# Kernel tuning notes

Hardware: AMD Instinct MI355X
Metric: run time of the kernel (lower is better)

## Reference

```python
import jax, jax.numpy as jnp
import numpy as np

B, Z, H, W, C = 1, 8, 60, 120, 192
HEADS = 6
HD = C // HEADS
WS = (2, 6, 12)
SS = (1, 3, 6)  # window_size//2 shifts
LAM = False
N = WS[0] * WS[1] * WS[2]  # 144 tokens per window
nZ, nH, nL = Z // WS[0], H // WS[1], W // WS[2]
TYPES = nZ * nH            # earth-specific bias window types (pl,lat absolute)
EPS = 1e-5


def _position_index():
    # Pangu earth-specific relative index: lon relative, pl/lat absolute pairs
    wz, wh, ww = WS
    c1 = np.stack(np.meshgrid(np.arange(wz), np.arange(wh), np.arange(ww), indexing='ij')).reshape(3, -1)
    c2 = np.stack(np.meshgrid(-np.arange(wz) * wz, -np.arange(wh) * wh, np.arange(ww), indexing='ij')).reshape(3, -1)
    d = (c1[:, :, None] - c2[:, None, :]).transpose(1, 2, 0)
    d[..., 2] += ww - 1
    d[..., 1] *= 2 * ww - 1
    d[..., 0] *= (2 * ww - 1) * wh * wh
    return d.sum(-1)  # (N, N)


def _attn_mask():
    # Swin-3D shifted-window mask; lon is periodic on the sphere (lam=False) -> unmasked
    img = np.zeros((Z, H, W), np.int32)
    def segs(w, s, masked):
        return [slice(0, -w), slice(-w, -s), slice(-s, None)] if masked else [slice(None)]
    cnt = 0
    for zs in segs(WS[0], SS[0], True):
        for hs in segs(WS[1], SS[1], True):
            for ls in segs(WS[2], SS[2], LAM):
                img[zs, hs, ls] = cnt
                cnt += 1
    m = img.reshape(nZ, WS[0], nH, WS[1], nL, WS[2]).transpose(0, 2, 4, 1, 3, 5).reshape(-1, N)
    return np.where(m[:, None, :] != m[:, :, None], -100.0, 0.0).astype(np.float32)  # (nZ*nH*nL, N, N)


POS_IDX = _position_index()
MASK = jnp.asarray(_attn_mask().reshape(TYPES, nL, 1, N, N))


def _layernorm(x, g, b):
    mu = x.mean(-1, keepdims=True)
    var = ((x - mu) ** 2).mean(-1, keepdims=True)
    return (x - mu) * jax.lax.rsqrt(var + EPS) * g + b


def setup_inputs() -> dict:
    key = jax.random.key(0)
    ks = jax.random.split(key, 8)
    f = lambda k, shape: jax.random.normal(k, shape, jnp.float32) * 0.02
    return {
        'x': jax.random.normal(ks[0], (B, Z * H * W, C), jnp.float32),
        'cond_embed': jax.random.normal(ks[1], (B, 6 * C), jnp.float32) * 0.1,
        'g1': jnp.ones((C,), jnp.float32), 'bt1': jnp.zeros((C,), jnp.float32),
        'w_qkv': f(ks[2], (C, 3 * C)), 'b_qkv': jnp.zeros((3 * C,), jnp.float32),
        'bias_table': f(ks[3], ((2 * WS[2] - 1) * WS[1] ** 2 * WS[0] ** 2, TYPES, HEADS)),
        'w_proj': f(ks[4], (C, C)), 'b_proj': jnp.zeros((C,), jnp.float32),
        'g2': jnp.ones((C,), jnp.float32), 'bt2': jnp.zeros((C,), jnp.float32),
        'w_fc1': f(ks[5], (C, 4 * C)), 'b_fc1': jnp.zeros((4 * C,), jnp.float32),
        'w_fc2': f(ks[6], (4 * C, C)), 'b_fc2': jnp.zeros((C,), jnp.float32),
    }


def reference(x, cond_embed, g1, bt1, w_qkv, b_qkv, bias_table, w_proj, b_proj,
              g2, bt2, w_fc1, b_fc1, w_fc2, b_fc2):
    shortcut = x
    sh_msa, sc_msa, gt_msa, sh_mlp, sc_mlp, gt_mlp = jnp.split(cond_embed, 6, axis=1)
    h = _layernorm(x, g1, bt1)
    h = h * (1 + sc_msa[:, None, :]) + sh_msa[:, None, :]          # AdaLN modulate
    h = h.reshape(B, Z, H, W, C)
    h = jnp.roll(h, (-SS[0], -SS[1], -SS[2]), axis=(1, 2, 3))     # shifted window
    # window partition -> (B*nZ*nH*nL, N, C)
    hw = h.reshape(B, nZ, WS[0], nH, WS[1], nL, WS[2], C)
    hw = hw.transpose(0, 1, 3, 5, 2, 4, 6, 7).reshape(-1, N, C)
    qkv = (hw @ w_qkv + b_qkv).reshape(-1, N, 3, HEADS, HD)
    q, k, v = qkv[:, :, 0], qkv[:, :, 1], qkv[:, :, 2]
    attn = jnp.einsum('bnhd,bmhd->bhnm', q * (HD ** -0.5), k)      # (B_, heads, N, N)
    bias = bias_table[POS_IDX].transpose(2, 3, 0, 1)               # (types, heads, N, N)
    attn = attn.reshape(B, TYPES, nL, HEADS, N, N)
    attn = attn + bias[None, :, None] + MASK[None]
    attn = jax.nn.softmax(attn, axis=-1).reshape(-1, HEADS, N, N)
    out = jnp.einsum('bhnm,bmhd->bnhd', attn, v).reshape(-1, N, C)
    out = out @ w_proj + b_proj
    # reverse window partition + roll back
    h = out.reshape(B, nZ, nH, nL, WS[0], WS[1], WS[2], C)
    h = h.transpose(0, 1, 4, 2, 5, 3, 6, 7).reshape(B, Z, H, W, C)
    h = jnp.roll(h, (SS[0], SS[1], SS[2]), axis=(1, 2, 3)).reshape(B, Z * H * W, C)
    y = shortcut + gt_msa[:, None, :] * h
    mlp_in = _layernorm(y, g2, bt2) * (1 + sc_mlp[:, None, :]) + sh_mlp[:, None, :]
    mlp_out = jax.nn.gelu(mlp_in @ w_fc1 + b_fc1, approximate=False) @ w_fc2 + b_fc2
    return y + gt_mlp[:, None, :] * mlp_out
```

## Files before the change

kernel.cpp:

```cpp
#include <hip/hip_runtime.h>
#include <hip/hip_bf16.h>
#include <cmath>

typedef short short8 __attribute__((ext_vector_type(8)));
typedef short short4v __attribute__((ext_vector_type(4)));
typedef float f32x4 __attribute__((ext_vector_type(4)));
typedef __hip_bfloat16 bf16;

static __device__ __forceinline__ float bf2f(bf16 v) { return __bfloat162float(v); }
static __device__ __forceinline__ bf16 f2bf(float v) { return __float2bfloat16(v); }
static __device__ __forceinline__ short bfbits(float v) {
    bf16 t = f2bf(v); return *reinterpret_cast<short*>(&t);
}
static __device__ __forceinline__ float sbits2f(short s) {
    unsigned int u = ((unsigned int)(unsigned short)s) << 16;
    float f; __builtin_memcpy(&f, &u, 4); return f;
}
static __device__ __forceinline__ float ldin(const void* p, size_t i, bool f32) {
    return f32 ? reinterpret_cast<const float*>(p)[i]
               : bf2f(reinterpret_cast<const bf16*>(p)[i]);
}
static __device__ __forceinline__ bool sniff_f32(const void* g1) {
    return reinterpret_cast<const unsigned short*>(g1)[0] == 0;
}

__global__ __launch_bounds__(256) void k_pre(
    const void* __restrict__ w0, const void* __restrict__ w1,
    const void* __restrict__ w2, const void* __restrict__ w3,
    bf16* __restrict__ Bt,
    const void* __restrict__ x, const void* __restrict__ cond,
    const void* __restrict__ g1, const void* __restrict__ bt1,
    bf16* __restrict__ hw, const void* __restrict__ btab,
    bf16* __restrict__ bm)
{
    bool f32 = sniff_f32(g1);
    int bb = blockIdx.x, tid = threadIdx.x;
    if (bb < 1728) {
        int e = bb * 256 + tid;
        const void* W; bf16* dst; int i, N, K;
        if (e < 110592)        { W = w0; dst = Bt;          i = e;          N = 576; K = 192; }
        else if (e < 147456)   { W = w1; dst = Bt + 110592; i = e - 110592; N = 192; K = 192; }
        else if (e < 294912)   { W = w2; dst = Bt + 147456; i = e - 147456; N = 768; K = 192; }
        else                   { W = w3; dst = Bt + 294912; i = e - 294912; N = 192; K = 768; }
        int k = i / N, n = i % N;
        dst[(size_t)n * K + k] = f2bf(ldin(W, i, f32));
        return;
    }
    if (bb < 1968) {
        int tb = bb - 1728;
        int type = tb / 6, head = tb % 6;
        int iz = type / 10, ih = type % 10;
        bf16* out = bm + (size_t)tb * 20736;
        for (int e = tid; e < 20736; e += 256) {
            int r = e & 3, l = (e >> 2) & 63, f = e >> 8;
            int nt = f % 9, w = f / 9;
            int i = w * 16 + (l >> 4) * 4 + r, j = nt * 16 + (l & 15);
            int a1 = i / 72, b1 = (i / 12) % 6, c1 = i % 12;
            int a2 = j / 72, b2 = (j / 12) % 6, c2 = j % 12;
            int pidx = ((a1 + 2 * a2) * 36 + (b1 + 6 * b2)) * 23 + (c1 - c2 + 11);
            float b = ldin(btab, (size_t)pidx * 240 + type * 6 + head, f32);
            int zi = iz * 2 + a1, hi = ih * 6 + b1;
            int zj = iz * 2 + a2, hj = ih * 6 + b2;
            int ri = (zi < 6 ? 0 : (zi < 7 ? 1 : 2)) * 3 + (hi < 54 ? 0 : (hi < 57 ? 1 : 2));
            int rj = (zj < 6 ? 0 : (zj < 7 ? 1 : 2)) * 3 + (hj < 54 ? 0 : (hj < 57 ? 1 : 2));
            if (ri != rj) b -= 100.0f;
            out[e] = f2bf(b);
        }
        return;
    }
    int t = (bb - 1968) * 4 + (tid >> 6);
    int lane = tid & 63;
    float v[3];
#pragma unroll
    for (int e = 0; e < 3; e++) v[e] = ldin(x, (size_t)t * 192 + lane + 64 * e, f32);
    float s = v[0] + v[1] + v[2];
#pragma unroll
    for (int off = 32; off; off >>= 1) s += __shfl_xor(s, off);
    float mu = s * (1.0f / 192.0f);
    float sq = 0.f;
#pragma unroll
    for (int e = 0; e < 3; e++) { float d = v[e] - mu; sq += d * d; }
#pragma unroll
    for (int off = 32; off; off >>= 1) sq += __shfl_xor(sq, off);
    float rs = rsqrtf(sq * (1.0f / 192.0f) + 1e-5f);

    int z = t / 7200, rem = t % 7200, hy = rem / 120, wx = rem % 120;
    int zr = (z + 7) & 7, hr = (hy + 57) % 60, wr = (wx + 114) % 120;
    int widx = ((zr >> 1) * 10 + hr / 6) * 10 + wr / 12;
    int n = ((zr & 1) * 6 + hr % 6) * 12 + wr % 12;
    bf16* dst = hw + ((size_t)widx * 144 + n) * 192;
#pragma unroll
    for (int e = 0; e < 3; e++) {
        int c = lane + 64 * e;
        float hv = (v[e] - mu) * rs * ldin(g1, c, f32) + ldin(bt1, c, f32);
        float o = hv * (1.0f + ldin(cond, 192 + c, f32)) + ldin(cond, c, f32);
        dst[c] = f2bf(o);
    }
}

__global__ __launch_bounds__(256) void k_gemm4(
    const bf16* __restrict__ A, const bf16* __restrict__ Bt,
    const void* __restrict__ bias, void* __restrict__ C,
    int Mrows, int N, int K,
    const void* __restrict__ g1)
{
    __shared__ short Bs[64 * 200];
    bool f32 = sniff_f32(g1);
    int tid = threadIdx.x;
    int wave = tid >> 6, lane = tid & 63, col16 = lane & 15, quad = lane >> 4;
    int nbase = blockIdx.x * 64;
    int mwave = blockIdx.y * 128 + wave * 32;

    f32x4 acc[2][4];
#pragma unroll
    for (int mi = 0; mi < 2; mi++)
#pragma unroll
        for (int nj = 0; nj < 4; nj++) acc[mi][nj] = (f32x4){0.f, 0.f, 0.f, 0.f};

    const short* aptr[2];
#pragma unroll
    for (int mi = 0; mi < 2; mi++) {
        int row = mwave + mi * 16 + col16;
        if (row >= Mrows) row = Mrows - 1;
        aptr[mi] = reinterpret_cast<const short*>(A) + (size_t)row * K + quad * 8;
    }

    for (int k0 = 0; k0 < K; k0 += 192) {
        if (k0) __syncthreads();
        short8 breg[6];
#pragma unroll
        for (int tt = 0; tt < 6; tt++) {
            int idx = tt * 256 + tid;
            int row = idx / 24, q = idx % 24;
            breg[tt] = *reinterpret_cast<const short8*>(
                Bt + (size_t)(nbase + row) * K + k0 + q * 8);
        }
        short8 af[2][6];
#pragma unroll
        for (int mi = 0; mi < 2; mi++)
#pragma unroll
            for (int kc = 0; kc < 6; kc++)
                af[mi][kc] = *reinterpret_cast<const short8*>(aptr[mi] + k0 + kc * 32);
#pragma unroll
        for (int tt = 0; tt < 6; tt++) {
            int idx = tt * 256 + tid;
            int row = idx / 24, q = idx % 24;
            *reinterpret_cast<short8*>(&Bs[row * 200 + q * 8]) = breg[tt];
        }
        __syncthreads();
#pragma unroll
        for (int kc = 0; kc < 6; kc++) {
            short8 bfrag[4];
#pragma unroll
            for (int nj = 0; nj < 4; nj++)
                bfrag[nj] = *reinterpret_cast<const short8*>(
                    &Bs[(nj * 16 + col16) * 200 + kc * 32 + quad * 8]);
#pragma unroll
            for (int mi = 0; mi < 2; mi++)
#pragma unroll
                for (int nj = 0; nj < 4; nj++)
                    acc[mi][nj] = __builtin_amdgcn_mfma_f32_16x16x32_bf16(
                        af[mi][kc], bfrag[nj], acc[mi][nj], 0, 0, 0);
        }
    }

    float bv[4];
#pragma unroll
    for (int nj = 0; nj < 4; nj++) bv[nj] = ldin(bias, nbase + nj * 16 + col16, f32);
    __syncthreads();

    short* Ss = Bs + wave * (32 * 72);
#pragma unroll
    for (int mi = 0; mi < 2; mi++)
#pragma unroll
        for (int nj = 0; nj < 4; nj++)
#pragma unroll
            for (int r = 0; r < 4; r++) {
                float v = acc[mi][nj][r] + bv[nj];
                Ss[(mi * 16 + quad * 4 + r) * 72 + nj * 16 + col16] = bfbits(v);
            }
    __syncthreads();
#pragma unroll
    for (int t = 0; t < 4; t++) {
        int rowl = t * 8 + (lane >> 3);
        int c0 = (lane & 7) * 8;
        short8 vv = *reinterpret_cast<const short8*>(&Ss[rowl * 72 + c0]);
        int rr = mwave + rowl;
        *reinterpret_cast<short8*>(
            &reinterpret_cast<short*>(C)[(size_t)rr * N + nbase + c0]) = vv;
    }
}

__global__ __launch_bounds__(576, 7) void k_fattn(
    const bf16* __restrict__ hw, const bf16* __restrict__ BtQ,
    const void* __restrict__ bqkv, const bf16* __restrict__ bm,
    bf16* __restrict__ aout, const void* __restrict__ g1)
{
    __shared__ short R[144 * 148];
    __shared__ short Vt[32 * 148];
    short* Bs = R;
    short* Qs = R;
    short* Ks = R + 5760;
    short* Ps = R;

    bool f32 = sniff_f32(g1);
    int b = blockIdx.x;
    int xcd = b & 7, idx = b >> 3;
    int widx = xcd * 50 + idx / 6, head = idx % 6;
    int type = widx / 10;
    int tid = threadIdx.x, wave = tid >> 6, lane = tid & 63;
    int col16 = lane & 15, quad = lane >> 4;
    f32x4 zero = (f32x4){0.f, 0.f, 0.f, 0.f};

    const short* bt = reinterpret_cast<const short*>(BtQ);
#pragma unroll
    for (int tt = 0; tt < 4; tt++) {
        int e = tt * 576 + tid;
        int row = e / 24, q = e % 24;
        int g = (row >> 5) * 192 + head * 32 + (row & 31);
        *reinterpret_cast<short8*>(&Bs[row * 200 + q * 8]) =
            *reinterpret_cast<const short8*>(bt + (size_t)g * 192 + q * 8);
    }
    const short* ap = reinterpret_cast<const short*>(hw)
        + ((size_t)widx * 144 + wave * 16 + col16) * 192 + quad * 8;
    short8 af[6];
#pragma unroll
    for (int kc = 0; kc < 6; kc++) af[kc] = *reinterpret_cast<const short8*>(ap + kc * 32);
    const short* bmb = reinterpret_cast<const short*>(bm) + (size_t)(type * 6 + head) * 20736;
    float brow[9][4];
#pragma unroll
    for (int nt = 0; nt < 9; nt++) {
        short4v bbv = *reinterpret_cast<const short4v*>(bmb + (((wave * 9 + nt) << 6) + lane) * 4);
#pragma unroll
        for (int r = 0; r < 4; r++) brow[nt][r] = sbits2f(bbv[r]);
    }
    f32x4 acc[6];
#pragma unroll
    for (int nj = 0; nj < 6; nj++) acc[nj] = zero;
    __syncthreads();

#pragma unroll
    for (int kc = 0; kc < 6; kc++) {
#pragma unroll
        for (int nj = 0; nj < 6; nj++) {
            short8 bfrag = *reinterpret_cast<const short8*>(
                &Bs[(nj * 16 + col16) * 200 + kc * 32 + quad * 8]);
            acc[nj] = __builtin_amdgcn_mfma_f32_16x16x32_bf16(af[kc], bfrag, acc[nj], 0, 0, 0);
        }
    }
    __syncthreads();
#pragma unroll
    for (int nj = 0; nj < 6; nj++) {
        float bv = ldin(bqkv, (size_t)((nj >> 1) * 192 + head * 32 + (nj & 1) * 16 + col16), f32);
        int d = (nj & 1) * 16 + col16;
#pragma unroll
        for (int r = 0; r < 4; r++) {
            int i = wave * 16 + quad * 4 + r;
            float v = acc[nj][r] + bv;
            if (nj < 2)      Qs[i * 40 + d] = bfbits(v * 0.17677669529663687f);
            else if (nj < 4) Ks[i * 40 + d] = bfbits(v);
            else             Vt[d * 148 + i] = bfbits(v);
        }
    }
    __syncthreads();

    short8 qfrag = *reinterpret_cast<const short8*>(&Qs[(wave * 16 + col16) * 40 + quad * 8]);
    f32x4 accs[9];
#pragma unroll
    for (int nt = 0; nt < 9; nt++) {
        short8 kfrag = *reinterpret_cast<const short8*>(&Ks[(nt * 16 + col16) * 40 + quad * 8]);
        accs[nt] = __builtin_amdgcn_mfma_f32_16x16x32_bf16(qfrag, kfrag, zero, 0, 0, 0);
    }
    __syncthreads();
    float rowm[4] = {-1e30f, -1e30f, -1e30f, -1e30f};
#pragma unroll
    for (int nt = 0; nt < 9; nt++) {
#pragma unroll
        for (int r = 0; r < 4; r++) {
            float v = accs[nt][r] + brow[nt][r];
            accs[nt][r] = v;
            rowm[r] = fmaxf(rowm[r], v);
        }
    }
#pragma unroll
    for (int r = 0; r < 4; r++)
#pragma unroll
        for (int off = 8; off; off >>= 1) rowm[r] = fmaxf(rowm[r], __shfl_xor(rowm[r], off));
    float rsum[4] = {0.f, 0.f, 0.f, 0.f};
#pragma unroll
    for (int nt = 0; nt < 9; nt++) {
#pragma unroll
        for (int r = 0; r < 4; r++) {
            float p = __expf(accs[nt][r] - rowm[r]);
            accs[nt][r] = p;
            rsum[r] += p;
        }
    }
#pragma unroll
    for (int r = 0; r < 4; r++)
#pragma unroll
        for (int off = 8; off; off >>= 1) rsum[r] += __shfl_xor(rsum[r], off);
    float inv[4];
#pragma unroll
    for (int r = 0; r < 4; r++) inv[r] = 1.0f / rsum[r];

#pragma unroll
    for (int nt = 0; nt < 9; nt++) {
#pragma unroll
        for (int r = 0; r < 4; r++) {
            int i = wave * 16 + quad * 4 + r;
            Ps[i * 148 + nt * 16 + col16] = bfbits(accs[nt][r] * inv[r]);
        }
    }
    __syncthreads();

    f32x4 acco[2];
    acco[0] = zero; acco[1] = zero;
#pragma unroll
    for (int kc = 0; kc < 5; kc++) {
        short8 pa = {0, 0, 0, 0, 0, 0, 0, 0};
        if (kc < 4 || quad < 2)
            pa = *reinterpret_cast<const short8*>(
                &Ps[(wave * 16 + col16) * 148 + kc * 32 + quad * 8]);
#pragma unroll
        for (int dt = 0; dt < 2; dt++) {
            short8 vb = {0, 0, 0, 0, 0, 0, 0, 0};
            if (kc < 4 || quad < 2)
                vb = *reinterpret_cast<const short8*>(
                    &Vt[(dt * 16 + col16) * 148 + kc * 32 + quad * 8]);
            acco[dt] = __builtin_amdgcn_mfma_f32_16x16x32_bf16(pa, vb, acco[dt], 0, 0, 0);
        }
    }
    __syncthreads();
    short* Os = &Ps[wave * 16 * 148];
#pragma unroll
    for (int dt = 0; dt < 2; dt++)
#pragma unroll
        for (int r = 0; r < 4; r++)
            Os[(quad * 4 + r) * 40 + dt * 16 + col16] = bfbits(acco[dt][r]);
    __syncthreads();
    {
        int rowl = lane >> 2, c0 = (lane & 3) * 8;
        short8 ov = *reinterpret_cast<const short8*>(&Os[rowl * 40 + c0]);
        *reinterpret_cast<short8*>(
            reinterpret_cast<short*>(aout)
            + ((size_t)widx * 144 + wave * 16 + rowl) * 192 + head * 32 + c0) = ov;
    }
}

__global__ __launch_bounds__(256) void k_ln2(
    const void* __restrict__ x, const void* __restrict__ cond,
    const void* __restrict__ g2, const void* __restrict__ bt2,
    const bf16* __restrict__ proj, bf16* __restrict__ y,
    bf16* __restrict__ mlpin, const void* __restrict__ g1)
{
    bool f32 = sniff_f32(g1);
    int t = blockIdx.x * 4 + (threadIdx.x >> 6);
    int lane = threadIdx.x & 63;
    int z = t / 7200, rem = t % 7200, hy = rem / 120, wx = rem % 120;
    int zr = (z + 7) & 7, hr = (hy + 57) % 60, wr = (wx + 114) % 120;
    int widx = ((zr >> 1) * 10 + hr / 6) * 10 + wr / 12;
    int n = ((zr & 1) * 6 + hr % 6) * 12 + wr % 12;
    const bf16* pr = proj + ((size_t)widx * 144 + n) * 192;
    float v[3];
#pragma unroll
    for (int e = 0; e < 3; e++) {
        int c = lane + 64 * e;
        v[e] = ldin(x, (size_t)t * 192 + c, f32) + ldin(cond, 384 + c, f32) * bf2f(pr[c]);
        y[(size_t)t * 192 + c] = f2bf(v[e]);
    }
    float s = v[0] + v[1] + v[2];
#pragma unroll
    for (int off = 32; off; off >>= 1) s += __shfl_xor(s, off);
    float mu = s * (1.0f / 192.0f);
    float sq = 0.f;
#pragma unroll
    for (int e = 0; e < 3; e++) { float d = v[e] - mu; sq += d * d; }
#pragma unroll
    for (int off = 32; off; off >>= 1) sq += __shfl_xor(sq, off);
    float rs = rsqrtf(sq * (1.0f / 192.0f) + 1e-5f);
#pragma unroll
    for (int e = 0; e < 3; e++) {
        int c = lane + 64 * e;
        float hv = (v[e] - mu) * rs * ldin(g2, c, f32) + ldin(bt2, c, f32);
        float o = hv * (1.0f + ldin(cond, 768 + c, f32)) + ldin(cond, 576 + c, f32);
        mlpin[(size_t)t * 192 + c] = f2bf(o);
    }
}

__global__ __launch_bounds__(256, 2) void k_mlp(
    const bf16* __restrict__ A, const bf16* __restrict__ B1t,
    const bf16* __restrict__ B2t, const void* __restrict__ b1,
    const void* __restrict__ b2, const bf16* __restrict__ yres,
    const void* __restrict__ cond, float* __restrict__ out,
    const void* __restrict__ g1)
{
    __shared__ short SL[12800 + 13824 + 9216];
    short* Bs1 = SL;
    short* Bs2 = SL + 12800;
    short* Hs  = SL + 26624;

    bool f32 = sniff_f32(g1);
    int tid = threadIdx.x;
    int wave = tid >> 6, lane = tid & 63, col16 = lane & 15, quad = lane >> 4;
    int mwave = blockIdx.x * 128 + wave * 32;

    const short* ap = reinterpret_cast<const short*>(A);
    short8 af[2][6];
#pragma unroll
    for (int mi = 0; mi < 2; mi++)
#pragma unroll
        for (int kc = 0; kc < 6; kc++)
            af[mi][kc] = *reinterpret_cast<const short8*>(
                ap + (size_t)(mwave + mi * 16 + col16) * 192 + kc * 32 + quad * 8);

    f32x4 zero = (f32x4){0.f, 0.f, 0.f, 0.f};
    f32x4 oacc[2][12];
#pragma unroll
    for (int mi = 0; mi < 2; mi++)
#pragma unroll
        for (int nj = 0; nj < 12; nj++) oacc[mi][nj] = zero;

    const short* b1p = reinterpret_cast<const short*>(B1t);
    const short* b2p = reinterpret_cast<const short*>(B2t);

    for (int hc = 0; hc < 12; hc++) {
        if (hc) __syncthreads();
#pragma unroll
        for (int tt = 0; tt < 6; tt++) {
            int idx = tt * 256 + tid;
            int row = idx / 24, q = idx % 24;
            *reinterpret_cast<short8*>(&Bs1[row * 200 + q * 8]) =
                *reinterpret_cast<const short8*>(
                    b1p + (size_t)(hc * 64 + row) * 192 + q * 8);
        }
#pragma unroll
        for (int tt = 0; tt < 6; tt++) {
            int idx = tt * 256 + tid;
            int row = idx >> 3, q = idx & 7;
            *reinterpret_cast<short8*>(&Bs2[row * 72 + q * 8]) =
                *reinterpret_cast<const short8*>(
                    b2p + (size_t)row * 768 + hc * 64 + q * 8);
        }
        __syncthreads();

        f32x4 hacc[2][4];
#pragma unroll
        for (int mi = 0; mi < 2; mi++)
#pragma unroll
            for (int nj = 0; nj < 4; nj++) hacc[mi][nj] = zero;
#pragma unroll
        for (int kc = 0; kc < 6; kc++) {
#pragma unroll
            for (int nj = 0; nj < 4; nj++) {
                short8 bfrag = *reinterpret_cast<const short8*>(
                    &Bs1[(nj * 16 + col16) * 200 + kc * 32 + quad * 8]);
#pragma unroll
                for (int mi = 0; mi < 2; mi++)
                    hacc[mi][nj] = __builtin_amdgcn_mfma_f32_16x16x32_bf16(
                        af[mi][kc], bfrag, hacc[mi][nj], 0, 0, 0);
            }
        }
        float b1v[4];
#pragma unroll
        for (int nj = 0; nj < 4; nj++)
            b1v[nj] = ldin(b1, (size_t)(hc * 64 + nj * 16 + col16), f32);
#pragma unroll
        for (int mi = 0; mi < 2; mi++)
#pragma unroll
            for (int nj = 0; nj < 4; nj++)
#pragma unroll
                for (int r = 0; r < 4; r++) {
                    float v = hacc[mi][nj][r] + b1v[nj];
                    v = 0.5f * v * (1.0f + erff(v * 0.70710678118654752f));
                    Hs[(wave * 32 + mi * 16 + quad * 4 + r) * 72 + nj * 16 + col16] = bfbits(v);
                }
        __syncthreads();
        short8 hf[2][2];
#pragma unroll
        for (int mi = 0; mi < 2; mi++)
#pragma unroll
            for (int kc = 0; kc < 2; kc++)
                hf[mi][kc] = *reinterpret_cast<const short8*>(
                    &Hs[(wave * 32 + mi * 16 + col16) * 72 + kc * 32 + quad * 8]);
#pragma unroll
        for (int kc = 0; kc < 2; kc++) {
#pragma unroll
            for (int nj = 0; nj < 12; nj++) {
                short8 bfrag = *reinterpret_cast<const short8*>(
                    &Bs2[(nj * 16 + col16) * 72 + kc * 32 + quad * 8]);
#pragma unroll
                for (int mi = 0; mi < 2; mi++)
                    oacc[mi][nj] = __builtin_amdgcn_mfma_f32_16x16x32_bf16(
                        hf[mi][kc], bfrag, oacc[mi][nj], 0, 0, 0);
            }
        }
    }

    float b2v[12];
#pragma unroll
    for (int nj = 0; nj < 12; nj++)
        b2v[nj] = ldin(b2, (size_t)(nj * 16 + col16), f32);
    float gte[3][4];
#pragma unroll
    for (int i = 0; i < 3; i++)
#pragma unroll
        for (int e = 0; e < 4; e++)
            gte[i][e] = ldin(cond, (size_t)(960 + ((lane & 15) + i * 16) * 4 + e), f32);
    __syncthreads();

    float* Ss = reinterpret_cast<float*>(SL) + wave * (16 * 196);
#pragma unroll
    for (int half = 0; half < 2; half++) {
        if (half) __syncthreads();
#pragma unroll
        for (int nj = 0; nj < 12; nj++)
#pragma unroll
            for (int r = 0; r < 4; r++)
                Ss[(quad * 4 + r) * 196 + nj * 16 + col16] = oacc[half][nj][r] + b2v[nj];
        __syncthreads();
#pragma unroll
        for (int p = 0; p < 4; p++) {
            int rowl = p * 4 + (lane >> 4);
            int rr = mwave + half * 16 + rowl;
#pragma unroll
            for (int i = 0; i < 3; i++) {
                int fcol = ((lane & 15) + i * 16) * 4;
                f32x4 sv = *reinterpret_cast<const f32x4*>(&Ss[rowl * 196 + fcol]);
                short4v yv = *reinterpret_cast<const short4v*>(
                    reinterpret_cast<const short*>(yres) + (size_t)rr * 192 + fcol);
                f32x4 ov;
#pragma unroll
                for (int e = 0; e < 4; e++) ov[e] = sbits2f(yv[e]) + gte[i][e] * sv[e];
                *reinterpret_cast<f32x4*>(&out[(size_t)rr * 192 + fcol]) = ov;
            }
        }
    }
}

extern "C" void kernel_launch(void* const* d_in, const int* in_sizes, int n_in,
                              void* d_out, int out_size, void* d_ws, size_t ws_size,
                              hipStream_t stream)
{
    const void* x     = d_in[0];
    const void* cond  = d_in[1];
    const void* g1    = d_in[2];
    const void* bt1   = d_in[3];
    const void* wqkv  = d_in[4];
    const void* bqkv  = d_in[5];
    const void* btab  = d_in[6];
    const void* wproj = d_in[7];
    const void* bproj = d_in[8];
    const void* g2    = d_in[9];
    const void* bt2   = d_in[10];
    const void* wfc1  = d_in[11];
    const void* bfc1  = d_in[12];
    const void* wfc2  = d_in[13];
    const void* bfc2  = d_in[14];

    char* ws = (char*)d_ws;
    bf16* hw     = (bf16*)(ws);
    bf16* projb  = (bf16*)(ws);
    bf16* attnb  = (bf16*)(ws + 22118400);
    bf16* yb     = (bf16*)(ws + 44236800);
    bf16* mlpin  = (bf16*)(ws + 66355200);
    bf16* bmb    = (bf16*)(ws + 88473600);
    bf16* BtAll  = (bf16*)(ws + 98426880);
    bf16* BtQ  = BtAll;
    bf16* BtP  = BtAll + 110592;
    bf16* BtF1 = BtAll + 147456;
    bf16* BtF2 = BtAll + 294912;

    k_pre<<<16368, 256, 0, stream>>>(wqkv, wproj, wfc1, wfc2, BtAll,
                                     x, cond, g1, bt1, hw, btab, bmb);
    k_fattn<<<2400, 576, 0, stream>>>(hw, BtQ, bqkv, bmb, attnb, g1);
    k_gemm4<<<dim3(3, 450), 256, 0, stream>>>(attnb, BtP, bproj, (void*)projb,
                                              57600, 192, 192, g1);
    k_ln2<<<14400, 256, 0, stream>>>(x, cond, g2, bt2, projb, yb, mlpin, g1);
    k_mlp<<<450, 256, 0, stream>>>(mlpin, BtF1, BtF2, bfc1, bfc2, yb, cond,
                                   (float*)d_out, g1);
}
```

Measured before the change: 344.5 us.

## Replace per-wave block barriers with fences and register-prefetch MLP weight tiles

Several __syncthreads barriers that guard shared-memory regions private to a single wave are replaced by __threadfence_block, removing block-wide stalls in the GEMM epilogue, the fused attention kernel, and the MLP kernel. The MLP kernel also prefetches the next hidden-chunk weight tiles for fc1 and fc2 into registers while the current chunk computes, so global load latency overlaps with MFMA work. This raises register pressure. It also relies on each wave only touching its own shared slice, plus the assumption that the fence is enough for intra-wave visibility. Any cross-wave aliasing, for example Ps rows in attention, could create races.

```diff
diff --git a/kernel.cpp b/kernel.cpp
--- a/kernel.cpp
+++ b/kernel.cpp
@@ -179,7 +179,7 @@
                 float v = acc[mi][nj][r] + bv[nj];
                 Ss[(mi * 16 + quad * 4 + r) * 72 + nj * 16 + col16] = bfbits(v);
             }
-    __syncthreads();
+    __threadfence_block();
 #pragma unroll
     for (int t = 0; t < 4; t++) {
         int rowl = t * 8 + (lane >> 3);
@@ -312,7 +312,7 @@
             Ps[i * 148 + nt * 16 + col16] = bfbits(accs[nt][r] * inv[r]);
         }
     }
-    __syncthreads();
+    __threadfence_block();
 
     f32x4 acco[2];
     acco[0] = zero; acco[1] = zero;
@@ -331,14 +331,14 @@
             acco[dt] = __builtin_amdgcn_mfma_f32_16x16x32_bf16(pa, vb, acco[dt], 0, 0, 0);
         }
     }
-    __syncthreads();
+    __threadfence_block();
     short* Os = &Ps[wave * 16 * 148];
 #pragma unroll
     for (int dt = 0; dt < 2; dt++)
 #pragma unroll
         for (int r = 0; r < 4; r++)
             Os[(quad * 4 + r) * 40 + dt * 16 + col16] = bfbits(acco[dt][r]);
-    __syncthreads();
+    __threadfence_block();
     {
         int rowl = lane >> 2, c0 = (lane & 3) * 8;
         short8 ov = *reinterpret_cast<const short8*>(&Os[rowl * 40 + c0]);
@@ -424,25 +424,39 @@
     const short* b1p = reinterpret_cast<const short*>(B1t);
     const short* b2p = reinterpret_cast<const short*>(B2t);
 
+    short8 p1[6], p2[6];
+#pragma unroll
+    for (int tt = 0; tt < 6; tt++) {
+        int idx = tt * 256 + tid;
+        int r1 = idx / 24, q1 = idx % 24;
+        p1[tt] = *reinterpret_cast<const short8*>(b1p + (size_t)r1 * 192 + q1 * 8);
+        int r2 = idx >> 3, q2 = idx & 7;
+        p2[tt] = *reinterpret_cast<const short8*>(b2p + (size_t)r2 * 768 + q2 * 8);
+    }
+
     for (int hc = 0; hc < 12; hc++) {
         if (hc) __syncthreads();
 #pragma unroll
         for (int tt = 0; tt < 6; tt++) {
             int idx = tt * 256 + tid;
-            int row = idx / 24, q = idx % 24;
-            *reinterpret_cast<short8*>(&Bs1[row * 200 + q * 8]) =
-                *reinterpret_cast<const short8*>(
-                    b1p + (size_t)(hc * 64 + row) * 192 + q * 8);
-        }
-#pragma unroll
-        for (int tt = 0; tt < 6; tt++) {
-            int idx = tt * 256 + tid;
-            int row = idx >> 3, q = idx & 7;
-            *reinterpret_cast<short8*>(&Bs2[row * 72 + q * 8]) =
-                *reinterpret_cast<const short8*>(
-                    b2p + (size_t)row * 768 + hc * 64 + q * 8);
+            int r1 = idx / 24, q1 = idx % 24;
+            *reinterpret_cast<short8*>(&Bs1[r1 * 200 + q1 * 8]) = p1[tt];
+            int r2 = idx >> 3, q2 = idx & 7;
+            *reinterpret_cast<short8*>(&Bs2[r2 * 72 + q2 * 8]) = p2[tt];
         }
         __syncthreads();
+        if (hc < 11) {
+#pragma unroll
+            for (int tt = 0; tt < 6; tt++) {
+                int idx = tt * 256 + tid;
+                int r1 = idx / 24, q1 = idx % 24;
+                p1[tt] = *reinterpret_cast<const short8*>(
+                    b1p + (size_t)((hc + 1) * 64 + r1) * 192 + q1 * 8);
+                int r2 = idx >> 3, q2 = idx & 7;
+                p2[tt] = *reinterpret_cast<const short8*>(
+                    b2p + (size_t)r2 * 768 + (hc + 1) * 64 + q2 * 8);
+            }
+        }
 
         f32x4 hacc[2][4];
 #pragma unroll
@@ -475,7 +489,7 @@
                     v = 0.5f * v * (1.0f + erff(v * 0.70710678118654752f));
                     Hs[(wave * 32 + mi * 16 + quad * 4 + r) * 72 + nj * 16 + col16] = bfbits(v);
                 }
-        __syncthreads();
+        __threadfence_block();
         short8 hf[2][2];
 #pragma unroll
         for (int mi = 0; mi < 2; mi++)
@@ -512,13 +526,13 @@
     float* Ss = reinterpret_cast<float*>(SL) + wave * (16 * 196);
 #pragma unroll
     for (int half = 0; half < 2; half++) {
-        if (half) __syncthreads();
+        if (half) __threadfence_block();
 #pragma unroll
         for (int nj = 0; nj < 12; nj++)
 #pragma unroll
             for (int r = 0; r < 4; r++)
                 Ss[(quad * 4 + r) * 196 + nj * 16 + col16] = oacc[half][nj][r] + b2v[nj];
-        __syncthreads();
+        __threadfence_block();
 #pragma unroll
         for (int p = 0; p < 4; p++) {
             int rowl = p * 4 + (lane >> 4);
```

New measurement: 366.1 us. 6.3% more time.

## Double-buffer MLP weight chunks via async global-to-LDS loads and relax barriers

Applied to the files above, without the earlier changes.

The MLP kernel now streams each fc1/fc2 weight chunk straight into LDS with global_load_lds. It uses two buffers so the next chunk loads while the current one feeds the MFMAs. The weight layout in LDS is changed to match the fragment order each lane reads. Several block-wide barriers in the GEMM, attention and MLP epilogues become block fences, on the basis that each wave only touches its own LDS region. In exchange, LDS use grows and the MLP launch bound drops to one block per SM. Correctness now depends on the barrier at the end of each loop iteration also waiting for the outstanding async loads.

```diff
diff --git a/kernel.cpp b/kernel.cpp
--- a/kernel.cpp
+++ b/kernel.cpp
@@ -22,6 +22,11 @@
 }
 static __device__ __forceinline__ bool sniff_f32(const void* g1) {
     return reinterpret_cast<const unsigned short*>(g1)[0] == 0;
+}
+static __device__ __forceinline__ void gld16(const void* g, void* l) {
+    __builtin_amdgcn_global_load_lds(
+        (const __attribute__((address_space(1))) unsigned int*)g,
+        (__attribute__((address_space(3))) unsigned int*)l, 16, 0, 0);
 }
 
 __global__ __launch_bounds__(256) void k_pre(
@@ -179,7 +184,7 @@
                 float v = acc[mi][nj][r] + bv[nj];
                 Ss[(mi * 16 + quad * 4 + r) * 72 + nj * 16 + col16] = bfbits(v);
             }
-    __syncthreads();
+    __threadfence_block();
 #pragma unroll
     for (int t = 0; t < 4; t++) {
         int rowl = t * 8 + (lane >> 3);
@@ -312,7 +317,7 @@
             Ps[i * 148 + nt * 16 + col16] = bfbits(accs[nt][r] * inv[r]);
         }
     }
-    __syncthreads();
+    __threadfence_block();
 
     f32x4 acco[2];
     acco[0] = zero; acco[1] = zero;
@@ -331,14 +336,14 @@
             acco[dt] = __builtin_amdgcn_mfma_f32_16x16x32_bf16(pa, vb, acco[dt], 0, 0, 0);
         }
     }
-    __syncthreads();
+    __threadfence_block();
     short* Os = &Ps[wave * 16 * 148];
 #pragma unroll
     for (int dt = 0; dt < 2; dt++)
 #pragma unroll
         for (int r = 0; r < 4; r++)
             Os[(quad * 4 + r) * 40 + dt * 16 + col16] = bfbits(acco[dt][r]);
-    __syncthreads();
+    __threadfence_block();
     {
         int rowl = lane >> 2, c0 = (lane & 3) * 8;
         short8 ov = *reinterpret_cast<const short8*>(&Os[rowl * 40 + c0]);
@@ -388,23 +393,24 @@
     }
 }
 
-__global__ __launch_bounds__(256, 2) void k_mlp(
+__global__ __launch_bounds__(256, 1) void k_mlp(
     const bf16* __restrict__ A, const bf16* __restrict__ B1t,
     const bf16* __restrict__ B2t, const void* __restrict__ b1,
     const void* __restrict__ b2, const bf16* __restrict__ yres,
     const void* __restrict__ cond, float* __restrict__ out,
     const void* __restrict__ g1)
 {
-    __shared__ short SL[12800 + 13824 + 9216];
-    short* Bs1 = SL;
-    short* Bs2 = SL + 12800;
-    short* Hs  = SL + 26624;
+    __shared__ short SL[58368];
+    short* Hs = SL + 49152;
 
     bool f32 = sniff_f32(g1);
     int tid = threadIdx.x;
     int wave = tid >> 6, lane = tid & 63, col16 = lane & 15, quad = lane >> 4;
     int mwave = blockIdx.x * 128 + wave * 32;
 
+    const short* b1p = reinterpret_cast<const short*>(B1t);
+    const short* b2p = reinterpret_cast<const short*>(B2t);
+
     const short* ap = reinterpret_cast<const short*>(A);
     short8 af[2][6];
 #pragma unroll
@@ -421,28 +427,35 @@
 #pragma unroll
         for (int nj = 0; nj < 12; nj++) oacc[mi][nj] = zero;
 
-    const short* b1p = reinterpret_cast<const short*>(B1t);
-    const short* b2p = reinterpret_cast<const short*>(B2t);
+#define ISSUE_CHUNK(hc, bufbase)                                               \
+    {                                                                          \
+        short* _b1 = (bufbase);                                                \
+        short* _b2 = (bufbase) + 12288;                                        \
+        _Pragma("unroll")                                                      \
+        for (int t = 0; t < 6; t++) {                                          \
+            int f = t * 4 + wave;                                              \
+            int kc = f >> 2, nj = f & 3;                                       \
+            gld16(b1p + (size_t)((hc) * 64 + nj * 16 + col16) * 192            \
+                      + kc * 32 + quad * 8,                                    \
+                  _b1 + f * 512);                                              \
+        }                                                                      \
+        _Pragma("unroll")                                                      \
+        for (int t = 0; t < 6; t++) {                                          \
+            int g = t * 4 + wave;                                              \
+            int kc = g / 12, nj = g % 12;                                      \
+            gld16(b2p + (size_t)(nj * 16 + col16) * 768                        \
+                      + (hc) * 64 + kc * 32 + quad * 8,                        \
+                  _b2 + g * 512);                                              \
+        }                                                                      \
+    }
+
+    ISSUE_CHUNK(0, SL);
+    __syncthreads();
 
     for (int hc = 0; hc < 12; hc++) {
-        if (hc) __syncthreads();
-#pragma unroll
-        for (int tt = 0; tt < 6; tt++) {
-            int idx = tt * 256 + tid;
-            int row = idx / 24, q = idx % 24;
-            *reinterpret_cast<short8*>(&Bs1[row * 200 + q * 8]) =
-                *reinterpret_cast<const short8*>(
-                    b1p + (size_t)(hc * 64 + row) * 192 + q * 8);
-        }
-#pragma unroll
-        for (int tt = 0; tt < 6; tt++) {
-            int idx = tt * 256 + tid;
-            int row = idx >> 3, q = idx & 7;
-            *reinterpret_cast<short8*>(&Bs2[row * 72 + q * 8]) =
-                *reinterpret_cast<const short8*>(
-                    b2p + (size_t)row * 768 + hc * 64 + q * 8);
-        }
-        __syncthreads();
+        short* cb = SL + (hc & 1) * 24576;
+        short* nb = SL + ((hc & 1) ^ 1) * 24576;
+        if (hc < 11) ISSUE_CHUNK(hc + 1, nb);
 
         f32x4 hacc[2][4];
 #pragma unroll
@@ -454,7 +467,7 @@
 #pragma unroll
             for (int nj = 0; nj < 4; nj++) {
                 short8 bfrag = *reinterpret_cast<const short8*>(
-                    &Bs1[(nj * 16 + col16) * 200 + kc * 32 + quad * 8]);
+                    &cb[((kc << 2) + nj) * 512 + lane * 8]);
 #pragma unroll
                 for (int mi = 0; mi < 2; mi++)
                     hacc[mi][nj] = __builtin_amdgcn_mfma_f32_16x16x32_bf16(
@@ -475,7 +488,8 @@
                     v = 0.5f * v * (1.0f + erff(v * 0.70710678118654752f));
                     Hs[(wave * 32 + mi * 16 + quad * 4 + r) * 72 + nj * 16 + col16] = bfbits(v);
                 }
-        __syncthreads();
+        asm volatile("s_waitcnt lgkmcnt(0)" ::: "memory");
+        __builtin_amdgcn_sched_barrier(0);
         short8 hf[2][2];
 #pragma unroll
         for (int mi = 0; mi < 2; mi++)
@@ -488,14 +502,16 @@
 #pragma unroll
             for (int nj = 0; nj < 12; nj++) {
                 short8 bfrag = *reinterpret_cast<const short8*>(
-                    &Bs2[(nj * 16 + col16) * 72 + kc * 32 + quad * 8]);
+                    &cb[12288 + (kc * 12 + nj) * 512 + lane * 8]);
 #pragma unroll
                 for (int mi = 0; mi < 2; mi++)
                     oacc[mi][nj] = __builtin_amdgcn_mfma_f32_16x16x32_bf16(
                         hf[mi][kc], bfrag, oacc[mi][nj], 0, 0, 0);
             }
         }
-    }
+        __syncthreads();
+    }
+#undef ISSUE_CHUNK
 
     float b2v[12];
 #pragma unroll
@@ -507,18 +523,17 @@
 #pragma unroll
         for (int e = 0; e < 4; e++)
             gte[i][e] = ldin(cond, (size_t)(960 + ((lane & 15) + i * 16) * 4 + e), f32);
-    __syncthreads();
 
     float* Ss = reinterpret_cast<float*>(SL) + wave * (16 * 196);
 #pragma unroll
     for (int half = 0; half < 2; half++) {
-        if (half) __syncthreads();
+        if (half) __threadfence_block();
 #pragma unroll
         for (int nj = 0; nj < 12; nj++)
 #pragma unroll
             for (int r = 0; r < 4; r++)
                 Ss[(quad * 4 + r) * 196 + nj * 16 + col16] = oacc[half][nj][r] + b2v[nj];
-        __syncthreads();
+        __threadfence_block();
 #pragma unroll
         for (int p = 0; p < 4; p++) {
             int rowl = p * 4 + (lane >> 4);
```

Result: slower. 374.6 us (+8.7%).
